# Performance work log

Hardware: AMD Instinct MI355X
Metric: run time of the kernel (lower is better)

The kernel has to match this reference:

```python
import math
import jax, jax.numpy as jnp
import numpy as np

DIM_IN = 2048
DIM_OUT = 2048
BLOCK = 128
N_BLOCKS = 256
SPARSITY = 0.1
BATCH = 8192


def setup_inputs() -> dict:
    key = jax.random.key(0)
    k1, k2, k3, k4, k5 = jax.random.split(key, 5)
    x = jax.random.normal(k1, (BATCH, DIM_IN), dtype=jnp.float32)
    weight = jax.random.normal(k2, (DIM_IN, DIM_OUT), dtype=jnp.float32) * (1.0 / math.sqrt(DIM_IN))
    bias = jax.random.normal(k3, (DIM_OUT,), dtype=jnp.float32) * 0.01
    gate_w = jax.random.normal(k4, (DIM_IN, N_BLOCKS), dtype=jnp.float32) * (1.0 / math.sqrt(DIM_IN))
    gate_b = jax.random.normal(k5, (N_BLOCKS,), dtype=jnp.float32) * 0.01
    return {"x": x, "weight": weight, "bias": bias, "gate_w": gate_w, "gate_b": gate_b}


def _sparsify1d(g):
    # k-th largest kept per row; threshold, mask, renormalize (Sparsify1D)
    n = g.shape[-1]
    k = int(math.ceil(SPARSITY * n))
    topval = jax.lax.top_k(g, k)[0][:, -1:]          # (B, 1) k-th largest value
    res = jnp.where(g >= topval, g, jnp.zeros_like(g))
    return res / (jnp.sum(res, axis=-1, keepdims=True) / n)


def reference(x, weight, bias, gate_w, gate_b):
    B = x.shape[0]
    s = DIM_IN // BLOCK                               # 16 block-rows/cols
    # gate network: Linear -> Sparsify1D
    g = _sparsify1d(x @ gate_w + gate_b)              # (B, s*s)
    gb = g.reshape(B, s, s)                           # (B, s_in, s_out)
    xb = x.reshape(B, s, BLOCK)                       # (B, s_in, block)
    Wb = weight.reshape(s, BLOCK, s, BLOCK)           # (s_in, block, s_out, block)
    # gated block matrix-vector multiply:
    # y[b,q,n] = sum_{p,m} g[b,p,q] * x[b,p,m] * W[p,m,q,n]
    y = jnp.einsum('bpq,bpm,pmqn->bqn', gb, xb, Wb)
    return y.reshape(B, DIM_OUT) + bias
```

## Files before the change

kernel.cpp:

```cpp
#include <hip/hip_runtime.h>
#include <hip/hip_bf16.h>
#include <stdint.h>

#define BATCH  8192
#define DIN    2048
#define DOUT   2048
#define NB     256
#define KSEL   26

typedef __attribute__((ext_vector_type(4))) float f32x4;
typedef __attribute__((ext_vector_type(8))) __bf16 bf16x8;
typedef __attribute__((ext_vector_type(8))) unsigned short u16x8;
typedef __attribute__((ext_vector_type(4))) unsigned short u16x4;

__device__ __forceinline__ float bf2f(unsigned short u){
  union { unsigned int i; float f; } v; v.i = ((unsigned int)u) << 16; return v.f;
}
__device__ __forceinline__ unsigned short f2bf(float f){
  union { float f; unsigned int i; } v; v.f = f;
  unsigned int x = v.i;
  return (unsigned short)((x + 0x7FFFu + ((x >> 16) & 1u)) >> 16);
}
__device__ __forceinline__ unsigned short f2bf_c(float f){
  __bf16 b = (__bf16)f;
  union { __bf16 b; unsigned short u; } v; v.b = b; return v.u;
}

__global__ __launch_bounds__(256) void conv_wt(const float* __restrict__ w, unsigned short* __restrict__ wt)
{
  __shared__ float tl[64][65];
  const int k0 = blockIdx.x * 64;
  const int n0 = blockIdx.y * 64;
  const int c  = threadIdx.x & 63;
  const int r4 = threadIdx.x >> 6;
  #pragma unroll
  for (int i = 0; i < 16; i++){
    const int r = r4 * 16 + i;
    tl[r][c] = w[(size_t)(k0 + r) * DOUT + n0 + c];
  }
  __syncthreads();
  #pragma unroll
  for (int i = 0; i < 16; i++){
    const int n = r4 * 16 + i;
    wt[(size_t)(n0 + n) * DIN + k0 + c] = f2bf(tl[c][n]);
  }
}

__global__ __launch_bounds__(256) void gate_gemm(
    const float* __restrict__ x, const float* __restrict__ gw,
    float* __restrict__ part, unsigned short* __restrict__ xb)
{
  __shared__ float xT[32][36];
  __shared__ float wT[32][260];
  const int b0 = blockIdx.x * 32;
  const int ks = blockIdx.y;
  const int t  = threadIdx.x;
  const int ct = t & 31;
  const int rt = t >> 5;

  f32x4 acc0[4], acc1[4];
  #pragma unroll
  for (int i = 0; i < 4; i++){ acc0[i] = (f32x4)0.0f; acc1[i] = (f32x4)0.0f; }

  const int sr  = t >> 3;
  const int sk  = (t & 7) * 4;
  const int wk  = (t >> 6) * 8;
  const int wc4 = (t & 63) * 4;

  const int koff = ks * 1024;
  for (int kc = 0; kc < 1024; kc += 32){
    {
      const size_t gi = (size_t)(b0 + sr) * DIN + koff + kc + sk;
      f32x4 a = *(const f32x4*)&x[gi];
      u16x4 ob;
      #pragma unroll
      for (int j = 0; j < 4; j++) ob[j] = f2bf_c(a[j]);
      *(u16x4*)&xb[gi] = ob;
      #pragma unroll
      for (int j = 0; j < 4; j++) xT[sk + j][sr] = a[j];
    }
    {
      #pragma unroll
      for (int i = 0; i < 8; i++){
        const int k = wk + i;
        *(f32x4*)&wT[k][wc4] = *(const f32x4*)&gw[(size_t)(koff + kc + k) * NB + wc4];
      }
    }
    __syncthreads();
    #pragma unroll 8
    for (int k = 0; k < 32; k++){
      f32x4 xv  = *(const f32x4*)&xT[k][rt * 4];
      f32x4 wv0 = *(const f32x4*)&wT[k][ct * 4];
      f32x4 wv1 = *(const f32x4*)&wT[k][ct * 4 + 128];
      #pragma unroll
      for (int i = 0; i < 4; i++){
        acc0[i] += xv[i] * wv0;
        acc1[i] += xv[i] * wv1;
      }
    }
    __syncthreads();
  }
  float* dst = part + (size_t)ks * BATCH * NB;
  #pragma unroll
  for (int i = 0; i < 4; i++){
    const int row = b0 + rt * 4 + i;
    *(f32x4*)&dst[(size_t)row * NB + ct * 4]       = acc0[i];
    *(f32x4*)&dst[(size_t)row * NB + ct * 4 + 128] = acc1[i];
  }
}

__global__ __launch_bounds__(256) void topk(float* __restrict__ part, const float* __restrict__ gb)
{
  const int lane = threadIdx.x & 63;
  const int row  = blockIdx.x * 4 + (threadIdx.x >> 6);
  f32x4* p0 = (f32x4*)&part[(size_t)row * NB];
  const f32x4* p1 = (const f32x4*)&part[(size_t)(BATCH + row) * NB];
  const f32x4* gbv = (const f32x4*)gb;
  f32x4 v = p0[lane] + p1[lane] + gbv[lane];

  const float NEG = -3.402823466e38f;
  float w0 = v[0], w1 = v[1], w2 = v[2], w3 = v[3];
  float thr = 0.f;
  for (int it = 0; it < KSEL; it++){
    float lm = fmaxf(fmaxf(w0, w1), fmaxf(w2, w3));
    float wm = lm;
    #pragma unroll
    for (int off = 32; off; off >>= 1) wm = fmaxf(wm, __shfl_xor(wm, off, 64));
    unsigned long long ball = __ballot(lm == wm);
    int first = __ffsll(ball) - 1;
    if (lane == first){
      if      (w0 == wm) w0 = NEG;
      else if (w1 == wm) w1 = NEG;
      else if (w2 == wm) w2 = NEG;
      else               w3 = NEG;
    }
    thr = wm;
  }
  float s = 0.f;
  #pragma unroll
  for (int j = 0; j < 4; j++) s += (v[j] >= thr) ? v[j] : 0.f;
  #pragma unroll
  for (int off = 32; off; off >>= 1) s += __shfl_xor(s, off, 64);
  const float d = s * (1.0f / NB);
  f32x4 o;
  #pragma unroll
  for (int j = 0; j < 4; j++) o[j] = (v[j] >= thr) ? v[j] / d : 0.f;
  p0[lane] = o;
}

__global__ __launch_bounds__(256) void main_gemm(
    const unsigned short* __restrict__ xb,
    const unsigned short* __restrict__ wt,
    const float* __restrict__ g,
    const float* __restrict__ bias,
    float* __restrict__ out)
{
  __shared__ unsigned short xa[128][72];
  __shared__ unsigned short wb[128][72];
  __shared__ float gl[128 * 17];

  const int q    = blockIdx.x;
  const int b0   = blockIdx.y * 128;
  const int t    = threadIdx.x;
  const int lane = t & 63;
  const int wid  = t >> 6;
  const int wr   = (wid >> 1) * 64;
  const int wc   = (wid & 1) * 64;
  const int l15  = lane & 15;
  const int l4   = lane >> 4;

  for (int e = t; e < 128 * 16; e += 256){
    const int r = e >> 4, p = e & 15;
    gl[r * 17 + p] = g[(size_t)(b0 + r) * NB + p * 16 + q];
  }

  f32x4 acc[4][4];
  #pragma unroll
  for (int m = 0; m < 4; m++)
    #pragma unroll
    for (int n = 0; n < 4; n++) acc[m][n] = (f32x4)0.0f;

  const int row_s = t >> 1;
  const int half  = t & 1;

  for (int kp = 0; kp < 32; kp++){
    const int p = kp >> 1;
    __syncthreads();
    {
      const float gate = gl[row_s * 17 + p];
      const unsigned short* src = &xb[(size_t)(b0 + row_s) * DIN + kp * 64 + half * 32];
      unsigned short* dst = &xa[row_s][half * 32];
      #pragma unroll
      for (int c = 0; c < 4; c++){
        u16x8 u = *(const u16x8*)(src + c * 8);
        u16x8 o;
        #pragma unroll
        for (int j = 0; j < 8; j++) o[j] = f2bf_c(bf2f(u[j]) * gate);
        *(u16x8*)(dst + c * 8) = o;
      }
    }
    {
      const unsigned short* src = &wt[(size_t)(q * 128 + row_s) * DIN + kp * 64 + half * 32];
      unsigned short* dst = &wb[row_s][half * 32];
      #pragma unroll
      for (int c = 0; c < 4; c++)
        *(u16x8*)(dst + c * 8) = *(const u16x8*)(src + c * 8);
    }
    __syncthreads();
    #pragma unroll
    for (int ksi = 0; ksi < 2; ksi++){
      const int kk = ksi * 32 + l4 * 8;
      bf16x8 a[4], b[4];
      #pragma unroll
      for (int m = 0; m < 4; m++)
        a[m] = *(const bf16x8*)&xa[wr + m * 16 + l15][kk];
      #pragma unroll
      for (int n = 0; n < 4; n++)
        b[n] = *(const bf16x8*)&wb[wc + n * 16 + l15][kk];
      #pragma unroll
      for (int m = 0; m < 4; m++)
        #pragma unroll
        for (int n = 0; n < 4; n++)
          acc[m][n] = __builtin_amdgcn_mfma_f32_16x16x32_bf16(a[m], b[n], acc[m][n], 0, 0, 0);
    }
  }

  #pragma unroll
  for (int n = 0; n < 4; n++){
    const int col = q * 128 + wc + n * 16 + l15;
    const float bv = bias[col];
    #pragma unroll
    for (int m = 0; m < 4; m++){
      #pragma unroll
      for (int r = 0; r < 4; r++){
        const int row = b0 + wr + m * 16 + l4 * 4 + r;
        out[(size_t)row * DOUT + col] = acc[m][n][r] + bv;
      }
    }
  }
}

extern "C" void kernel_launch(void* const* d_in, const int* in_sizes, int n_in,
                              void* d_out, int out_size, void* d_ws, size_t ws_size,
                              hipStream_t stream)
{
  const float* x    = (const float*)d_in[0];
  const float* w    = (const float*)d_in[1];
  const float* bias = (const float*)d_in[2];
  const float* gw   = (const float*)d_in[3];
  const float* gb   = (const float*)d_in[4];
  float* out = (float*)d_out;

  float*          part = (float*)d_ws;
  unsigned short* wtb  = (unsigned short*)((char*)d_ws + (size_t)16 * 1024 * 1024);
  unsigned short* xbb  = (unsigned short*)((char*)d_ws + (size_t)24 * 1024 * 1024);

  conv_wt  <<<dim3(DIN / 64, DOUT / 64), 256, 0, stream>>>(w, wtb);
  gate_gemm<<<dim3(BATCH / 32, 2), 256, 0, stream>>>(x, gw, part, xbb);
  topk     <<<BATCH / 4, 256, 0, stream>>>(part, gb);
  main_gemm<<<dim3(16, BATCH / 128), 256, 0, stream>>>(xbb, wtb, part, bias, out);
}
```

Before: 269.2 us.

## Read gate weights directly from global memory instead of staging in LDS

New measurement: 312.9 us. 16.2% more time.

```diff
diff --git a/kernel.cpp b/kernel.cpp
--- a/kernel.cpp
+++ b/kernel.cpp
@@ -8,6 +8,7 @@
 #define NB     256
 #define KSEL   26
 
+typedef __attribute__((ext_vector_type(2))) float f32x2;
 typedef __attribute__((ext_vector_type(4))) float f32x4;
 typedef __attribute__((ext_vector_type(8))) __bf16 bf16x8;
 typedef __attribute__((ext_vector_type(8))) unsigned short u16x8;
@@ -51,24 +52,24 @@
     float* __restrict__ part, unsigned short* __restrict__ xb)
 {
   __shared__ float xT[32][36];
-  __shared__ float wT[32][260];
-  const int b0 = blockIdx.x * 32;
-  const int ks = blockIdx.y;
-  const int t  = threadIdx.x;
-  const int ct = t & 31;
-  const int rt = t >> 5;
-
-  f32x4 acc0[4], acc1[4];
-  #pragma unroll
-  for (int i = 0; i < 4; i++){ acc0[i] = (f32x4)0.0f; acc1[i] = (f32x4)0.0f; }
-
-  const int sr  = t >> 3;
-  const int sk  = (t & 7) * 4;
-  const int wk  = (t >> 6) * 8;
-  const int wc4 = (t & 63) * 4;
+  const int b0   = blockIdx.x * 32;
+  const int ks   = blockIdx.y;
+  const int t    = threadIdx.x;
+  const int lane = t & 63;
+  const int wv   = t >> 6;
+  const int rg   = (wv >> 1) * 16;
+  const int cb   = (wv & 1) * 128 + (lane << 1);
+
+  float acc[16][2];
+  #pragma unroll
+  for (int i = 0; i < 16; i++){ acc[i][0] = 0.f; acc[i][1] = 0.f; }
+
+  const int sr = t >> 3;
+  const int sk = (t & 7) * 4;
 
   const int koff = ks * 1024;
   for (int kc = 0; kc < 1024; kc += 32){
+    __syncthreads();
     {
       const size_t gi = (size_t)(b0 + sr) * DIN + koff + kc + sk;
       f32x4 a = *(const f32x4*)&x[gi];
@@ -79,33 +80,34 @@
       #pragma unroll
       for (int j = 0; j < 4; j++) xT[sk + j][sr] = a[j];
     }
-    {
-      #pragma unroll
-      for (int i = 0; i < 8; i++){
-        const int k = wk + i;
-        *(f32x4*)&wT[k][wc4] = *(const f32x4*)&gw[(size_t)(koff + kc + k) * NB + wc4];
+    __syncthreads();
+    const float* gwp = &gw[(size_t)(koff + kc) * NB + cb];
+    #pragma unroll 4
+    for (int k = 0; k < 32; k++){
+      f32x2 wvv = *(const f32x2*)(gwp + (size_t)k * NB);
+      f32x4 xv0 = *(const f32x4*)&xT[k][rg];
+      f32x4 xv1 = *(const f32x4*)&xT[k][rg + 4];
+      f32x4 xv2 = *(const f32x4*)&xT[k][rg + 8];
+      f32x4 xv3 = *(const f32x4*)&xT[k][rg + 12];
+      #pragma unroll
+      for (int j = 0; j < 4; j++){
+        acc[j][0]      = fmaf(xv0[j], wvv[0], acc[j][0]);
+        acc[j][1]      = fmaf(xv0[j], wvv[1], acc[j][1]);
+        acc[j + 4][0]  = fmaf(xv1[j], wvv[0], acc[j + 4][0]);
+        acc[j + 4][1]  = fmaf(xv1[j], wvv[1], acc[j + 4][1]);
+        acc[j + 8][0]  = fmaf(xv2[j], wvv[0], acc[j + 8][0]);
+        acc[j + 8][1]  = fmaf(xv2[j], wvv[1], acc[j + 8][1]);
+        acc[j + 12][0] = fmaf(xv3[j], wvv[0], acc[j + 12][0]);
+        acc[j + 12][1] = fmaf(xv3[j], wvv[1], acc[j + 12][1]);
       }
     }
-    __syncthreads();
-    #pragma unroll 8
-    for (int k = 0; k < 32; k++){
-      f32x4 xv  = *(const f32x4*)&xT[k][rt * 4];
-      f32x4 wv0 = *(const f32x4*)&wT[k][ct * 4];
-      f32x4 wv1 = *(const f32x4*)&wT[k][ct * 4 + 128];
-      #pragma unroll
-      for (int i = 0; i < 4; i++){
-        acc0[i] += xv[i] * wv0;
-        acc1[i] += xv[i] * wv1;
-      }
-    }
-    __syncthreads();
   }
   float* dst = part + (size_t)ks * BATCH * NB;
   #pragma unroll
-  for (int i = 0; i < 4; i++){
-    const int row = b0 + rt * 4 + i;
-    *(f32x4*)&dst[(size_t)row * NB + ct * 4]       = acc0[i];
-    *(f32x4*)&dst[(size_t)row * NB + ct * 4 + 128] = acc1[i];
+  for (int i = 0; i < 16; i++){
+    const int row = b0 + rg + i;
+    f32x2 o; o[0] = acc[i][0]; o[1] = acc[i][1];
+    *(f32x2*)&dst[(size_t)row * NB + cb] = o;
   }
 }
 
```
